# Performance work log

Measured on AMD Instinct MI355X. Metric: run time of the kernel, lower is better.

## Reference

```python
import math
import jax, jax.numpy as jnp
import numpy as np

HIDDEN = 1024
HEADS = 16
HEAD_DIM = HIDDEN // HEADS
PRIME = 7
MAX_ITERS = 10
ENT_THRESH = 0.2
PRIME_SCALE = 1.0 / math.sqrt(PRIME * HEAD_DIM)
EPS = 1e-6


def setup_inputs() -> dict:
    key = jax.random.key(0)
    ks = jax.random.split(key, 6)
    B, S = 2, 2048
    w = 0.02
    return {
        "hidden_states": jax.random.normal(ks[0], (B, S, HIDDEN), jnp.float32),
        "q_w": jax.random.normal(ks[1], (HIDDEN, HIDDEN), jnp.float32) * w,
        "q_b": jnp.zeros((HIDDEN,), jnp.float32),
        "k_w": jax.random.normal(ks[2], (HIDDEN, HIDDEN), jnp.float32) * w,
        "k_b": jnp.zeros((HIDDEN,), jnp.float32),
        "v_w": jax.random.normal(ks[3], (HIDDEN, HIDDEN), jnp.float32) * w,
        "v_b": jnp.zeros((HIDDEN,), jnp.float32),
        "o_w": jax.random.normal(ks[4], (HIDDEN, HIDDEN), jnp.float32) * w,
        "o_b": jnp.zeros((HIDDEN,), jnp.float32),
        "attention_mask": jnp.ones((B, S), jnp.int32),
    }


def _split_heads(x):
    B, S, _ = x.shape
    return x.reshape(B, S, HEADS, HEAD_DIM).transpose(0, 2, 1, 3)


def reference(hidden_states, q_w, q_b, k_w, k_b, v_w, v_b, o_w, o_b, attention_mask):
    B, S, _ = hidden_states.shape
    # projections (torch Linear: x @ W^T + b)
    q = _split_heads(hidden_states @ q_w.T + q_b) * PRIME_SCALE  # [B,H,S,hd]
    k = _split_heads(hidden_states @ k_w.T + k_b)
    v = _split_heads(hidden_states @ v_w.T + v_b)

    scores = jnp.einsum("bhqd,bhkd->bhqk", q, k)  # [B,H,S,S]
    mask = attention_mask[:, None, None, :]
    scores = jnp.where(mask == 0, -jnp.inf, scores)
    attn = jax.nn.softmax(scores, axis=-1)  # dropout p=0 (eval)

    base = jnp.einsum("bhqk,bhkd->bhqd", attn, v)  # attention_weights @ v

    # entropy of the (fixed) attention weights: [B,H]
    entropy = -jnp.sum(attn * jnp.log(attn + EPS), axis=-1).mean(axis=-1)
    avg_entropy = entropy.mean()

    # loop never changes attn, so entropy is constant: either break at i=1 or run all
    full = base
    for i in range(1, MAX_ITERS):
        blend = 1.0 / (1.0 + math.exp(-i / MAX_ITERS))          # sigmoid(i/max)
        res_scale = 0.5 + 0.5 * blend                            # resonance scale
        full = (1.0 - blend) * full + blend * (res_scale * base)

    out_heads = jnp.where(avg_entropy < ENT_THRESH, base, full)  # [B,H,S,hd]

    merged = out_heads.transpose(0, 2, 1, 3).reshape(B, S, HIDDEN)
    return merged @ o_w.T + o_b
```

## Files before the change

### kernel.cpp

```cpp
#include <hip/hip_runtime.h>
#include <hip/hip_bf16.h>
#include <stdint.h>


#define PRIME_SCALE 0.047245559126654356f
#define LOG2E       1.4426950408889634f
#define LN2         0.6931471805599453f
#define QSCALE      (PRIME_SCALE * LOG2E)
#define BLEND_C     0.85096556f

#if __has_builtin(__builtin_amdgcn_exp2f)
#define EXP2(x) __builtin_amdgcn_exp2f(x)
#else
#define EXP2(x) exp2f(x)
#endif

typedef __attribute__((ext_vector_type(8))) short short8;
typedef __attribute__((ext_vector_type(4))) float f32x4;

__device__ __forceinline__ unsigned short f2bf(float x) {
    union { float f; unsigned int u; } v; v.f = x;
    unsigned int r = (v.u + 0x7fffu + ((v.u >> 16) & 1u)) >> 16;
    return (unsigned short)r;
}
__device__ __forceinline__ unsigned short f2bf_fast(float x) {
    union { float f; unsigned int u; } v; v.f = x;
    return (unsigned short)((v.u + 0x8000u) >> 16);
}
__device__ __forceinline__ float bf2f(unsigned short x) {
    union { unsigned int u; float f; } v; v.u = ((unsigned int)x) << 16;
    return v.f;
}
__device__ __forceinline__ unsigned cvtpk_bf16(float lo, float hi) {
    unsigned r;
    asm("v_cvt_pk_bf16_f32 %0, %1, %2" : "=v"(r) : "v"(lo), "v"(hi));
    return r;
}

__device__ __forceinline__ void glds16(const unsigned short* g, unsigned short* l) {
    __builtin_amdgcn_global_load_lds((const __attribute__((address_space(1))) unsigned int*)g,
                                     (__attribute__((address_space(3))) unsigned int*)l,
                                     16, 0, 0);
}

__global__ void zero_out_f32(float* p, int n) {
    int i = blockIdx.x * 256 + threadIdx.x;
    if (i < n) p[i] = 0.f;
}

__global__ __launch_bounds__(256) void cvt5(
    const float* __restrict__ s0, const float* __restrict__ s1, const float* __restrict__ s2,
    const float* __restrict__ s3, const float* __restrict__ s4,
    unsigned short* __restrict__ d0, unsigned short* __restrict__ d1, unsigned short* __restrict__ d2,
    unsigned short* __restrict__ d3, unsigned short* __restrict__ d4, float* entp)
{
    if (blockIdx.x == 0 && threadIdx.x == 0) entp[0] = 0.f;
    unsigned int i = blockIdx.x * 256 + threadIdx.x;
    const float* s; unsigned short* d; unsigned int off;
    if (i < (1u << 20)) { s = s0; d = d0; off = i; }
    else {
        unsigned int j = i - (1u << 20);
        unsigned int sel = j >> 18; off = j & 0x3FFFFu;
        s = sel == 0 ? s1 : sel == 1 ? s2 : sel == 2 ? s3 : s4;
        d = sel == 0 ? d1 : sel == 1 ? d2 : sel == 2 ? d3 : d4;
    }
    float4 v = ((const float4*)s)[off];
    ushort4 p; p.x = f2bf(v.x); p.y = f2bf(v.y); p.z = f2bf(v.z); p.w = f2bf(v.w);
    ((ushort4*)d)[off] = p;
}

__global__ __launch_bounds__(256) void gemm_qkv(
    const unsigned short* __restrict__ hsb,
    const unsigned short* __restrict__ qwb, const unsigned short* __restrict__ kwb,
    const unsigned short* __restrict__ vwb,
    const float* __restrict__ qb, const float* __restrict__ kb, const float* __restrict__ vb,
    unsigned short* __restrict__ Qo, unsigned short* __restrict__ Ko, unsigned short* __restrict__ Vto)
{
    const int bid = blockIdx.x;
    const int op = bid >> 8, local = bid & 255;
    const unsigned short *A, *B; const float* bias; unsigned short* C;
    int m0, n0, ldc, biasRow; float scale;
    if (op == 0)      { A = hsb; B = qwb; bias = qb; C = Qo;  m0 = (local >> 3) * 128; n0 = (local & 7) * 128;  ldc = 1024; biasRow = 0; scale = QSCALE; }
    else if (op == 1) { A = hsb; B = kwb; bias = kb; C = Ko;  m0 = (local >> 3) * 128; n0 = (local & 7) * 128;  ldc = 1024; biasRow = 0; scale = 1.f; }
    else              { A = vwb; B = hsb; bias = vb; C = Vto; m0 = (local >> 5) * 128; n0 = (local & 31) * 128; ldc = 4096; biasRow = 1; scale = 1.f; }

    __shared__ unsigned short As[128 * 32];
    __shared__ unsigned short Bs[128 * 32];
    const int t = threadIdx.x, lane = t & 63, w = t >> 6;
    const int quad = lane >> 4, l15 = lane & 15;
    const int wr = (w >> 1) * 64, wc = (w & 1) * 64;
    const int srow = lane >> 2, scol = (lane & 3) * 8;

    f32x4 acc[4][4];
#pragma unroll
    for (int i = 0; i < 4; ++i)
#pragma unroll
        for (int j = 0; j < 4; ++j) acc[i][j] = (f32x4){0.f, 0.f, 0.f, 0.f};

    for (int kk = 0; kk < 32; ++kk) {
        const int k0 = kk * 32;
#pragma unroll
        for (int j = 0; j < 2; ++j) {
            int row = (w * 2 + j) * 16 + srow;
            glds16(&A[(size_t)(m0 + row) * 1024 + k0 + scol], &As[(w * 2 + j) * 512]);
            glds16(&B[(size_t)(n0 + row) * 1024 + k0 + scol], &Bs[(w * 2 + j) * 512]);
        }
        __syncthreads();
        short8 af[4], bf[4];
#pragma unroll
    for (int mt = 0; mt < 4; ++mt) af[mt] = *(const short8*)&As[(wr + mt * 16 + l15) * 32 + quad * 8];
#pragma unroll
        for (int nt = 0; nt < 4; ++nt) bf[nt] = *(const short8*)&Bs[(wc + nt * 16 + l15) * 32 + quad * 8];
#pragma unroll
        for (int mt = 0; mt < 4; ++mt)
#pragma unroll
            for (int nt = 0; nt < 4; ++nt)
                acc[mt][nt] = __builtin_amdgcn_mfma_f32_16x16x32_bf16(af[mt], bf[nt], acc[mt][nt], 0, 0, 0);
        __syncthreads();
    }
#pragma unroll
    for (int mt = 0; mt < 4; ++mt) {
#pragma unroll
        for (int nt = 0; nt < 4; ++nt) {
            int n = n0 + wc + nt * 16 + l15;
#pragma unroll
            for (int r = 0; r < 4; ++r) {
                int m = m0 + wr + mt * 16 + quad * 4 + r;
                float bval = biasRow ? bias[m] : bias[n];
                C[(size_t)m * ldc + n] = f2bf((acc[mt][nt][r] + bval) * scale);
            }
        }
    }
}


#define STAGE(KT, BUF) do {                                                         \
    int kn_ = (KT) * 64;                                                            \
    _Pragma("unroll")                                                               \
    for (int i_ = 0; i_ < 2; ++i_) {                                                \
        int row_ = w * 16 + i_ * 8 + r8;                                            \
        int c_ = ch8 ^ (row_ & 7);                                                  \
        glds16(&K[(size_t)(b * 2048 + kn_ + row_) * 1024 + h * 64 + c_ * 8],        \
               &Ks[BUF][(w * 16 + i_ * 8) * 64]);                                   \
        glds16(&Vt[(size_t)(h * 64 + row_) * 4096 + b * 2048 + kn_ + c_ * 8],       \
               &Vs[BUF][(w * 16 + i_ * 8) * 64]);                                   \
    }                                                                               \
} while (0)

#define QK_SOFTMAX(MASKED)                                                          \
    _Pragma("unroll")                                                               \
    for (int nt = 0; nt < 4; ++nt) {                                                \
        int krow = nt * 16 + l15;                                                   \
        short8 kf0 = *(const short8*)&Ks[cur][krow * 64 + ((quad ^ (krow & 7)) * 8)];       \
        short8 kf1 = *(const short8*)&Ks[cur][krow * 64 + (((quad + 4) ^ (krow & 7)) * 8)]; \
        f32x4 sv[2];                                                                \
        __builtin_amdgcn_s_setprio(1);                                              \
        _Pragma("unroll")                                                           \
        for (int st = 0; st < 2; ++st) {                                            \
            sv[st] = __builtin_amdgcn_mfma_f32_16x16x32_bf16(kf0, qa[st][0], (f32x4){0.f, 0.f, 0.f, 0.f}, 0, 0, 0); \
            sv[st] = __builtin_amdgcn_mfma_f32_16x16x32_bf16(kf1, qa[st][1], sv[st], 0, 0, 0); \
        }                                                                           \
        __builtin_amdgcn_s_setprio(0);                                              \
        unsigned mb = 0xFu;                                                         \
        if (MASKED) {                                                               \
            unsigned mw = (nt & 2) ? mwB : mwA;                                     \
            mb = (mw >> (((nt & 1) << 4) + (quad << 2))) & 0xFu;                    \
        }                                                                           \
        _Pragma("unroll")                                                           \
        for (int st = 0; st < 2; ++st) {                                            \
            float s0 = sv[st][0], s1 = sv[st][1], s2 = sv[st][2], s3 = sv[st][3];   \
            if (MASKED) {                                                           \
                s0 = (mb & 1u) ? s0 : -1.0e30f;                                     \
                s1 = (mb & 2u) ? s1 : -1.0e30f;                                     \
                s2 = (mb & 4u) ? s2 : -1.0e30f;                                     \
                s3 = (mb & 8u) ? s3 : -1.0e30f;                                     \
            }                                                                       \
            float p0 = EXP2(s0), p1 = EXP2(s1), p2 = EXP2(s2), p3 = EXP2(s3);       \
            l_r[st] += (p0 + p1) + (p2 + p3);                                       \
            T_r[st] += (p0 * s0 + p1 * s1) + (p2 * s2 + p3 * s3);                   \
            pk[nt][st][0] = cvtpk_bf16(p0, p1);                                     \
            pk[nt][st][1] = cvtpk_bf16(p2, p3);                                     \
        }                                                                           \
    }

__global__ __launch_bounds__(256, 2) void flash_split(
    const unsigned short* __restrict__ Q,
    const unsigned short* __restrict__ K,
    const unsigned short* __restrict__ Vt,
    const int* __restrict__ mask,
    unsigned short* __restrict__ O0, unsigned short* __restrict__ O1,
    float* __restrict__ lpart, float* __restrict__ Tpart)
{
    const int ww = ((blockIdx.x & 7) << 7) + (blockIdx.x >> 3);
    const int qt = ww & 15;
    const int pr = ww >> 4;
    const int bh = pr >> 1;
    const int z  = pr & 1;
    const int b = bh >> 4, h = bh & 15;
    const int t = threadIdx.x, lane = t & 63, w = t >> 6;
    const int quad = lane >> 4, l15 = lane & 15;
    const int r8 = lane >> 3, ch8 = lane & 7;
    const int kt0 = z * 16, kt1 = kt0 + 16;
    unsigned short* __restrict__ Opart = z ? O1 : O0;

    __shared__ __align__(16) unsigned short Ks[2][64 * 64];
    __shared__ __align__(16) unsigned short Vs[2][64 * 64];
    __shared__ unsigned int maskBits[64];

    short8 qa[2][2];
#pragma unroll
    for (int st = 0; st < 2; ++st) {
        size_t qrow = (size_t)(b * 2048 + qt * 128 + w * 32 + st * 16 + l15) * 1024 + h * 64;
        union { uint4 v; short8 s8; } u0, u1;
        u0.v = *(const uint4*)&Q[qrow + quad * 8];
        u1.v = *(const uint4*)&Q[qrow + 32 + quad * 8];
        qa[st][0] = u0.s8; qa[st][1] = u1.s8;
    }

    {
        const int4* mp = (const int4*)(mask + b * 2048 + t * 8);
        int4 a = mp[0], c = mp[1];
        unsigned bits = (unsigned)(a.x != 0)       | ((unsigned)(a.y != 0) << 1)
                      | ((unsigned)(a.z != 0) << 2) | ((unsigned)(a.w != 0) << 3)
                      | ((unsigned)(c.x != 0) << 4) | ((unsigned)(c.y != 0) << 5)
                      | ((unsigned)(c.z != 0) << 6) | ((unsigned)(c.w != 0) << 7);
        ((unsigned char*)maskBits)[t] = (unsigned char)bits;
    }

    STAGE(kt0, 0);
    STAGE(kt0 + 1, 1);

    float l_r[2] = {0.f, 0.f}, T_r[2] = {0.f, 0.f};
    f32x4 o_acc[2][4];
#pragma unroll
    for (int st = 0; st < 2; ++st)
#pragma unroll
        for (int nt = 0; nt < 4; ++nt) o_acc[st][nt] = (f32x4){0.f, 0.f, 0.f, 0.f};

    asm volatile("s_waitcnt lgkmcnt(0)" ::: "memory");
    asm volatile("s_waitcnt vmcnt(4)" ::: "memory");
    asm volatile("s_barrier" ::: "memory");

    for (int kt = kt0; kt < kt1; ++kt) {
        const int cur = kt & 1;
        unsigned mwA = maskBits[kt * 2], mwB = maskBits[kt * 2 + 1];

        unsigned pk[4][2][2];
        if ((mwA & mwB) == 0xFFFFFFFFu) {
            QK_SOFTMAX(0)
        } else {
            QK_SOFTMAX(1)
        }

#pragma unroll
        for (int ks = 0; ks < 2; ++ks) {
            short8 pa[2];
#pragma unroll
            for (int st = 0; st < 2; ++st) {
                unsigned a0 = pk[2 * ks][st][0], a1 = pk[2 * ks][st][1];
                unsigned b0 = pk[2 * ks + 1][st][0], b1 = pk[2 * ks + 1][st][1];
                asm("v_permlane32_swap_b32 %0, %1" : "+v"(a0), "+v"(b0));
                asm("v_permlane32_swap_b32 %0, %1" : "+v"(a1), "+v"(b1));
                asm("v_permlane16_swap_b32 %0, %1" : "+v"(a0), "+v"(b0));
                asm("v_permlane16_swap_b32 %0, %1" : "+v"(a1), "+v"(b1));
                union { unsigned u[4]; short8 s8; } uu;
                uu.u[0] = a0; uu.u[1] = a1; uu.u[2] = b0; uu.u[3] = b1;
                pa[st] = uu.s8;
            }
            __builtin_amdgcn_s_setprio(1);
#pragma unroll
            for (int nt = 0; nt < 4; ++nt) {
                int vrow = nt * 16 + l15;
                short8 vf = *(const short8*)&Vs[cur][vrow * 64 + ((((ks * 4 + quad)) ^ (vrow & 7)) * 8)];
#pragma unroll
                for (int st = 0; st < 2; ++st)
                    o_acc[st][nt] = __builtin_amdgcn_mfma_f32_16x16x32_bf16(pa[st], vf, o_acc[st][nt], 0, 0, 0);
            }
            __builtin_amdgcn_s_setprio(0);
        }

        if (kt < kt1 - 1) {
            asm volatile("s_barrier" ::: "memory");
            if (kt < kt1 - 2) {
                STAGE(kt + 2, cur);
                asm volatile("s_waitcnt vmcnt(4)" ::: "memory");
            } else {
                asm volatile("s_waitcnt vmcnt(0)" ::: "memory");
            }
            asm volatile("s_barrier" ::: "memory");
        }
    }

#pragma unroll
    for (int st = 0; st < 2; ++st) {
        float l = l_r[st], T = T_r[st];
        l += __shfl_xor(l, 16); T += __shfl_xor(T, 16);
        l += __shfl_xor(l, 32); T += __shfl_xor(T, 32);
        if (lane < 16) {
            int qrow = qt * 128 + w * 32 + st * 16 + l15;
            int li = z * 65536 + bh * 2048 + qrow;
            lpart[li] = l; Tpart[li] = T;
        }
#pragma unroll
        for (int r = 0; r < 4; ++r) {
            int mrow = b * 2048 + qt * 128 + w * 32 + st * 16 + quad * 4 + r;
#pragma unroll
            for (int nt = 0; nt < 4; ++nt)
                Opart[(size_t)mrow * 1024 + h * 64 + nt * 16 + l15] = f2bf_fast(o_acc[st][nt][r]);
        }
    }
}

__global__ __launch_bounds__(256) void combine_split(
    unsigned short* __restrict__ O0, const unsigned short* __restrict__ O1,
    const float* __restrict__ lpart)
{
    unsigned idx = blockIdx.x * 256 + threadIdx.x;
    int mrow = idx >> 8;
    int c4 = (idx & 255) << 2;
    int h = c4 >> 6;
    int b = mrow >> 11, qrow = mrow & 2047;
    int li = (b * 16 + h) * 2048 + qrow;
    float l = lpart[li] + lpart[65536 + li];
    float inv = 1.0f / l;

    ushort4 a = ((const ushort4*)O0)[idx];
    ushort4 c = ((const ushort4*)O1)[idx];
    ushort4 o;
    o.x = f2bf_fast((bf2f(a.x) + bf2f(c.x)) * inv);
    o.y = f2bf_fast((bf2f(a.y) + bf2f(c.y)) * inv);
    o.z = f2bf_fast((bf2f(a.z) + bf2f(c.z)) * inv);
    o.w = f2bf_fast((bf2f(a.w) + bf2f(c.w)) * inv);
    ((ushort4*)O0)[idx] = o;
}

__global__ __launch_bounds__(256) void entropy_k(
    const float* __restrict__ lpart, const float* __restrict__ Tpart,
    float* __restrict__ entp)
{
    __shared__ float wsum[4];
    int idx = blockIdx.x * 256 + threadIdx.x;
    float acc = 0.f;
#pragma unroll
    for (int i = 0; i < 4; ++i) {
        int r = idx * 4 + i;
        float l = lpart[r] + lpart[65536 + r];
        float T = Tpart[r] + Tpart[65536 + r];
        acc += __log2f(l) - T / l;
    }
    acc += __shfl_xor(acc, 1);
    acc += __shfl_xor(acc, 2);
    acc += __shfl_xor(acc, 4);
    acc += __shfl_xor(acc, 8);
    acc += __shfl_xor(acc, 16);
    acc += __shfl_xor(acc, 32);
    int lane = threadIdx.x & 63, w = threadIdx.x >> 6;
    if (lane == 0) wsum[w] = acc;
    __syncthreads();
    if (threadIdx.x == 0)
        atomicAdd(entp, LN2 * (wsum[0] + wsum[1] + wsum[2] + wsum[3]));
}

__global__ __launch_bounds__(256) void gemm_out_bf(
    const unsigned short* __restrict__ A, const unsigned short* __restrict__ Bw,
    const float* __restrict__ bias, const float* __restrict__ entp,
    float* __restrict__ C)
{
    const float avg = entp[0] * (1.0f / 65536.0f);
    const float scale = (avg < 0.2f) ? 1.0f : BLEND_C;

    const int m0 = blockIdx.x * 128;
    const int n0 = blockIdx.y * 64;
    __shared__ unsigned short As[128 * 32];
    __shared__ unsigned short Bs[64 * 32];
    const int t = threadIdx.x, lane = t & 63, w = t >> 6;
    const int quad = lane >> 4, l15 = lane & 15;
    const int wr = (w >> 1) * 64, wc = (w & 1) * 32;
    const int srow = lane >> 2, scol = (lane & 3) * 8;

    f32x4 acc[4][2];
#pragma unroll
    for (int i = 0; i < 4; ++i)
#pragma unroll
        for (int j = 0; j < 2; ++j) acc[i][j] = (f32x4){0.f, 0.f, 0.f, 0.f};

    for (int kk = 0; kk < 32; ++kk) {
        const int k0 = kk * 32;
#pragma unroll
        for (int j = 0; j < 2; ++j) {
            int row = (w * 2 + j) * 16 + srow;
            glds16(&A[(size_t)(m0 + row) * 1024 + k0 + scol], &As[(w * 2 + j) * 512]);
        }
        {
            int row = w * 16 + srow;
            glds16(&Bw[(size_t)(n0 + row) * 1024 + k0 + scol], &Bs[w * 512]);
        }
        __syncthreads();
        short8 af[4], bf[2];
#pragma unroll
        for (int mt = 0; mt < 4; ++mt) af[mt] = *(const short8*)&As[(wr + mt * 16 + l15) * 32 + quad * 8];
#pragma unroll
        for (int nt = 0; nt < 2; ++nt) bf[nt] = *(const short8*)&Bs[(wc + nt * 16 + l15) * 32 + quad * 8];
#pragma unroll
        for (int mt = 0; mt < 4; ++mt)
#pragma unroll
            for (int nt = 0; nt < 2; ++nt)
                acc[mt][nt] = __builtin_amdgcn_mfma_f32_16x16x32_bf16(af[mt], bf[nt], acc[mt][nt], 0, 0, 0);
        __syncthreads();
    }
#pragma unroll
    for (int mt = 0; mt < 4; ++mt) {
#pragma unroll
        for (int nt = 0; nt < 2; ++nt) {
            int n = n0 + wc + nt * 16 + l15;
#pragma unroll
            for (int r = 0; r < 4; ++r) {
                int m = m0 + wr + mt * 16 + quad * 4 + r;
                C[(size_t)m * 1024 + n] = scale * acc[mt][nt][r] + bias[n];
            }
        }
    }
}

extern "C" void kernel_launch(void* const* d_in, const int* in_sizes, int n_in,
                              void* d_out, int out_size, void* d_ws, size_t ws_size,
                              hipStream_t stream)
{
    const float* hs = (const float*)d_in[0];
    const float* qw = (const float*)d_in[1];
    const float* qb = (const float*)d_in[2];
    const float* kw = (const float*)d_in[3];
    const float* kb = (const float*)d_in[4];
    const float* vw = (const float*)d_in[5];
    const float* vb = (const float*)d_in[6];
    const float* ow = (const float*)d_in[7];
    const float* ob = (const float*)d_in[8];
    const int*   mask = (const int*)d_in[9];
    float* out = (float*)d_out;

    const size_t MB = 1024 * 1024;
    char* ws = (char*)d_ws;
    dim3 blk(256);

    if (ws_size >= 50 * MB) {
        unsigned short* hsb = (unsigned short*)(ws);
        unsigned short* Q   = (unsigned short*)(ws + 8 * MB);
        unsigned short* Kp  = (unsigned short*)(ws + 16 * MB);
        unsigned short* Vt  = (unsigned short*)(ws + 24 * MB);
        unsigned short* qwb = (unsigned short*)(ws + 32 * MB);
        unsigned short* kwb = (unsigned short*)(ws + 34 * MB);
        unsigned short* vwb = (unsigned short*)(ws + 36 * MB);
        unsigned short* owb = (unsigned short*)(ws + 38 * MB);
        float* entp         = (float*)(ws + 40 * MB);
        unsigned short* Op1 = (unsigned short*)(ws + 41 * MB);
        float* lpart        = (float*)(ws + 49 * MB);
        float* Tpart        = (float*)(ws + 49 * MB + 524288);
        unsigned short* Op0 = hsb;

        cvt5<<<dim3(8192), blk, 0, stream>>>(hs, qw, kw, vw, ow, hsb, qwb, kwb, vwb, owb, entp);
        gemm_qkv<<<dim3(768), blk, 0, stream>>>(hsb, qwb, kwb, vwb, qb, kb, vb, Q, Kp, Vt);
        flash_split<<<dim3(1024), blk, 0, stream>>>(Q, Kp, Vt, mask, Op0, Op1, lpart, Tpart);
        combine_split<<<dim3(4096), blk, 0, stream>>>(Op0, Op1, lpart);
        entropy_k<<<dim3(64), blk, 0, stream>>>(lpart, Tpart, entp);
        gemm_out_bf<<<dim3(32, 16), blk, 0, stream>>>(Op0, owb, ob, entp, out);
    } else {
        zero_out_f32<<<dim3((out_size + 255) / 256), blk, 0, stream>>>(out, out_size);
    }
}
```

Measured before the change: 206.1 us.

## Drop split-KV flash attention; fuse normalization and entropy into single-pass kernel

Replaces the two-way split over the key dimension with one flash kernel per query tile that walks all 32 key tiles. Softmax normalization and the per-row entropy reduction now happen inside that kernel, which removes the combine and entropy kernels and the partial-output round trips through global memory. The output-projection GEMM tile also grows from 128x64 to 128x128. The cost is half as many flash blocks (512), so there is less parallelism and a longer serial loop per block, plus more register pressure in the GEMM.

```diff
diff --git a/kernel.cpp b/kernel.cpp
--- a/kernel.cpp
+++ b/kernel.cpp
@@ -108,7 +108,7 @@
         __syncthreads();
         short8 af[4], bf[4];
 #pragma unroll
-    for (int mt = 0; mt < 4; ++mt) af[mt] = *(const short8*)&As[(wr + mt * 16 + l15) * 32 + quad * 8];
+        for (int mt = 0; mt < 4; ++mt) af[mt] = *(const short8*)&As[(wr + mt * 16 + l15) * 32 + quad * 8];
 #pragma unroll
         for (int nt = 0; nt < 4; ++nt) bf[nt] = *(const short8*)&Bs[(wc + nt * 16 + l15) * 32 + quad * 8];
 #pragma unroll
@@ -183,29 +183,26 @@
         }                                                                           \
     }
 
-__global__ __launch_bounds__(256, 2) void flash_split(
+__global__ __launch_bounds__(256, 2) void flash_full(
     const unsigned short* __restrict__ Q,
     const unsigned short* __restrict__ K,
     const unsigned short* __restrict__ Vt,
     const int* __restrict__ mask,
-    unsigned short* __restrict__ O0, unsigned short* __restrict__ O1,
-    float* __restrict__ lpart, float* __restrict__ Tpart)
+    unsigned short* __restrict__ O,
+    float* __restrict__ entp)
 {
-    const int ww = ((blockIdx.x & 7) << 7) + (blockIdx.x >> 3);
+    const int ww = ((blockIdx.x & 7) << 6) + (blockIdx.x >> 3);
     const int qt = ww & 15;
-    const int pr = ww >> 4;
-    const int bh = pr >> 1;
-    const int z  = pr & 1;
+    const int bh = ww >> 4;
     const int b = bh >> 4, h = bh & 15;
     const int t = threadIdx.x, lane = t & 63, w = t >> 6;
     const int quad = lane >> 4, l15 = lane & 15;
     const int r8 = lane >> 3, ch8 = lane & 7;
-    const int kt0 = z * 16, kt1 = kt0 + 16;
-    unsigned short* __restrict__ Opart = z ? O1 : O0;
 
     __shared__ __align__(16) unsigned short Ks[2][64 * 64];
     __shared__ __align__(16) unsigned short Vs[2][64 * 64];
     __shared__ unsigned int maskBits[64];
+    __shared__ float went[4];
 
     short8 qa[2][2];
 #pragma unroll
@@ -227,8 +224,8 @@
         ((unsigned char*)maskBits)[t] = (unsigned char)bits;
     }
 
-    STAGE(kt0, 0);
-    STAGE(kt0 + 1, 1);
+    STAGE(0, 0);
+    STAGE(1, 1);
 
     float l_r[2] = {0.f, 0.f}, T_r[2] = {0.f, 0.f};
     f32x4 o_acc[2][4];
@@ -241,7 +238,7 @@
     asm volatile("s_waitcnt vmcnt(4)" ::: "memory");
     asm volatile("s_barrier" ::: "memory");
 
-    for (int kt = kt0; kt < kt1; ++kt) {
+    for (int kt = 0; kt < 32; ++kt) {
         const int cur = kt & 1;
         unsigned mwA = maskBits[kt * 2], mwB = maskBits[kt * 2 + 1];
 
@@ -279,9 +276,9 @@
             __builtin_amdgcn_s_setprio(0);
         }
 
-        if (kt < kt1 - 1) {
+        if (kt < 31) {
             asm volatile("s_barrier" ::: "memory");
-            if (kt < kt1 - 2) {
+            if (kt < 30) {
                 STAGE(kt + 2, cur);
                 asm volatile("s_waitcnt vmcnt(4)" ::: "memory");
             } else {
@@ -291,74 +288,33 @@
         }
     }
 
+    float ent_acc = 0.f;
 #pragma unroll
     for (int st = 0; st < 2; ++st) {
         float l = l_r[st], T = T_r[st];
         l += __shfl_xor(l, 16); T += __shfl_xor(T, 16);
         l += __shfl_xor(l, 32); T += __shfl_xor(T, 32);
-        if (lane < 16) {
-            int qrow = qt * 128 + w * 32 + st * 16 + l15;
-            int li = z * 65536 + bh * 2048 + qrow;
-            lpart[li] = l; Tpart[li] = T;
-        }
+        ent_acc += __log2f(l) - T / l;
+        float inv[4];
+#pragma unroll
+        for (int r = 0; r < 4; ++r)
+            inv[r] = 1.0f / __shfl(l, quad * 4 + r);
 #pragma unroll
         for (int r = 0; r < 4; ++r) {
             int mrow = b * 2048 + qt * 128 + w * 32 + st * 16 + quad * 4 + r;
 #pragma unroll
             for (int nt = 0; nt < 4; ++nt)
-                Opart[(size_t)mrow * 1024 + h * 64 + nt * 16 + l15] = f2bf_fast(o_acc[st][nt][r]);
-        }
-    }
-}
-
-__global__ __launch_bounds__(256) void combine_split(
-    unsigned short* __restrict__ O0, const unsigned short* __restrict__ O1,
-    const float* __restrict__ lpart)
-{
-    unsigned idx = blockIdx.x * 256 + threadIdx.x;
-    int mrow = idx >> 8;
-    int c4 = (idx & 255) << 2;
-    int h = c4 >> 6;
-    int b = mrow >> 11, qrow = mrow & 2047;
-    int li = (b * 16 + h) * 2048 + qrow;
-    float l = lpart[li] + lpart[65536 + li];
-    float inv = 1.0f / l;
-
-    ushort4 a = ((const ushort4*)O0)[idx];
-    ushort4 c = ((const ushort4*)O1)[idx];
-    ushort4 o;
-    o.x = f2bf_fast((bf2f(a.x) + bf2f(c.x)) * inv);
-    o.y = f2bf_fast((bf2f(a.y) + bf2f(c.y)) * inv);
-    o.z = f2bf_fast((bf2f(a.z) + bf2f(c.z)) * inv);
-    o.w = f2bf_fast((bf2f(a.w) + bf2f(c.w)) * inv);
-    ((ushort4*)O0)[idx] = o;
-}
-
-__global__ __launch_bounds__(256) void entropy_k(
-    const float* __restrict__ lpart, const float* __restrict__ Tpart,
-    float* __restrict__ entp)
-{
-    __shared__ float wsum[4];
-    int idx = blockIdx.x * 256 + threadIdx.x;
-    float acc = 0.f;
-#pragma unroll
-    for (int i = 0; i < 4; ++i) {
-        int r = idx * 4 + i;
-        float l = lpart[r] + lpart[65536 + r];
-        float T = Tpart[r] + Tpart[65536 + r];
-        acc += __log2f(l) - T / l;
-    }
-    acc += __shfl_xor(acc, 1);
-    acc += __shfl_xor(acc, 2);
-    acc += __shfl_xor(acc, 4);
-    acc += __shfl_xor(acc, 8);
-    acc += __shfl_xor(acc, 16);
-    acc += __shfl_xor(acc, 32);
-    int lane = threadIdx.x & 63, w = threadIdx.x >> 6;
-    if (lane == 0) wsum[w] = acc;
+                O[(size_t)mrow * 1024 + h * 64 + nt * 16 + l15] = f2bf_fast(o_acc[st][nt][r] * inv[r]);
+        }
+    }
+    ent_acc += __shfl_xor(ent_acc, 1);
+    ent_acc += __shfl_xor(ent_acc, 2);
+    ent_acc += __shfl_xor(ent_acc, 4);
+    ent_acc += __shfl_xor(ent_acc, 8);
+    if (lane == 0) went[w] = ent_acc;
     __syncthreads();
-    if (threadIdx.x == 0)
-        atomicAdd(entp, LN2 * (wsum[0] + wsum[1] + wsum[2] + wsum[3]));
+    if (t == 0)
+        atomicAdd(entp, LN2 * (went[0] + went[1] + went[2] + went[3]));
 }
 
 __global__ __launch_bounds__(256) void gemm_out_bf(
@@ -370,19 +326,19 @@
     const float scale = (avg < 0.2f) ? 1.0f : BLEND_C;
 
     const int m0 = blockIdx.x * 128;
-    const int n0 = blockIdx.y * 64;
+    const int n0 = blockIdx.y * 128;
     __shared__ unsigned short As[128 * 32];
-    __shared__ unsigned short Bs[64 * 32];
+    __shared__ unsigned short Bs[128 * 32];
     const int t = threadIdx.x, lane = t & 63, w = t >> 6;
     const int quad = lane >> 4, l15 = lane & 15;
-    const int wr = (w >> 1) * 64, wc = (w & 1) * 32;
+    const int wr = (w >> 1) * 64, wc = (w & 1) * 64;
     const int srow = lane >> 2, scol = (lane & 3) * 8;
 
-    f32x4 acc[4][2];
+    f32x4 acc[4][4];
 #pragma unroll
     for (int i = 0; i < 4; ++i)
 #pragma unroll
-        for (int j = 0; j < 2; ++j) acc[i][j] = (f32x4){0.f, 0.f, 0.f, 0.f};
+        for (int j = 0; j < 4; ++j) acc[i][j] = (f32x4){0.f, 0.f, 0.f, 0.f};
 
     for (int kk = 0; kk < 32; ++kk) {
         const int k0 = kk * 32;
@@ -390,28 +346,25 @@
         for (int j = 0; j < 2; ++j) {
             int row = (w * 2 + j) * 16 + srow;
             glds16(&A[(size_t)(m0 + row) * 1024 + k0 + scol], &As[(w * 2 + j) * 512]);
-        }
-        {
-            int row = w * 16 + srow;
-            glds16(&Bw[(size_t)(n0 + row) * 1024 + k0 + scol], &Bs[w * 512]);
+            glds16(&Bw[(size_t)(n0 + row) * 1024 + k0 + scol], &Bs[(w * 2 + j) * 512]);
         }
         __syncthreads();
-        short8 af[4], bf[2];
+        short8 af[4], bf[4];
 #pragma unroll
         for (int mt = 0; mt < 4; ++mt) af[mt] = *(const short8*)&As[(wr + mt * 16 + l15) * 32 + quad * 8];
 #pragma unroll
-        for (int nt = 0; nt < 2; ++nt) bf[nt] = *(const short8*)&Bs[(wc + nt * 16 + l15) * 32 + quad * 8];
+        for (int nt = 0; nt < 4; ++nt) bf[nt] = *(const short8*)&Bs[(wc + nt * 16 + l15) * 32 + quad * 8];
 #pragma unroll
         for (int mt = 0; mt < 4; ++mt)
 #pragma unroll
-            for (int nt = 0; nt < 2; ++nt)
+            for (int nt = 0; nt < 4; ++nt)
                 acc[mt][nt] = __builtin_amdgcn_mfma_f32_16x16x32_bf16(af[mt], bf[nt], acc[mt][nt], 0, 0, 0);
         __syncthreads();
     }
 #pragma unroll
     for (int mt = 0; mt < 4; ++mt) {
 #pragma unroll
-        for (int nt = 0; nt < 2; ++nt) {
+        for (int nt = 0; nt < 4; ++nt) {
             int n = n0 + wc + nt * 16 + l15;
 #pragma unroll
             for (int r = 0; r < 4; ++r) {
@@ -452,17 +405,12 @@
         unsigned short* vwb = (unsigned short*)(ws + 36 * MB);
         unsigned short* owb = (unsigned short*)(ws + 38 * MB);
         float* entp         = (float*)(ws + 40 * MB);
-        unsigned short* Op1 = (unsigned short*)(ws + 41 * MB);
-        float* lpart        = (float*)(ws + 49 * MB);
-        float* Tpart        = (float*)(ws + 49 * MB + 524288);
-        unsigned short* Op0 = hsb;
+        unsigned short* O   = hsb;
 
         cvt5<<<dim3(8192), blk, 0, stream>>>(hs, qw, kw, vw, ow, hsb, qwb, kwb, vwb, owb, entp);
         gemm_qkv<<<dim3(768), blk, 0, stream>>>(hsb, qwb, kwb, vwb, qb, kb, vb, Q, Kp, Vt);
-        flash_split<<<dim3(1024), blk, 0, stream>>>(Q, Kp, Vt, mask, Op0, Op1, lpart, Tpart);
-        combine_split<<<dim3(4096), blk, 0, stream>>>(Op0, Op1, lpart);
-        entropy_k<<<dim3(64), blk, 0, stream>>>(lpart, Tpart, entp);
-        gemm_out_bf<<<dim3(32, 16), blk, 0, stream>>>(Op0, owb, ob, entp, out);
+        flash_full<<<dim3(512), blk, 0, stream>>>(Q, Kp, Vt, mask, O, entp);
+        gemm_out_bf<<<dim3(32, 8), blk, 0, stream>>>(O, owb, ob, entp, out);
     } else {
         zero_out_f32<<<dim3((out_size + 255) / 256), blk, 0, stream>>>(out, out_size);
     }
```

Measured after the change: 205.2 us. No clear change (-0.4%).
